# Kernel optimization log

Hardware: AMD Instinct MI355X
Metric: run time of the kernel (lower is better)

Reference implementation:

```python
import jax, jax.numpy as jnp
import numpy as np


def setup_inputs() -> dict:
    key = jax.random.key(0)
    ks = jax.random.split(key, 8)
    B, S, I, H = 64, 256, 1024, 1024
    stdv = 1.0 / np.sqrt(H)
    inputs = jax.random.normal(ks[0], (B, S, I), dtype=jnp.float32)
    h0 = jax.random.normal(ks[1], (1, B, H), dtype=jnp.float32)
    c0 = jax.random.normal(ks[2], (1, B, H), dtype=jnp.float32)
    # concatenated gate params in order (i, f, g, o), uniform(-stdv, stdv) like reset_weigths
    w_i = jax.random.uniform(ks[3], (4 * H, I), minval=-stdv, maxval=stdv, dtype=jnp.float32)
    w_h = jax.random.uniform(ks[4], (4 * H, H), minval=-stdv, maxval=stdv, dtype=jnp.float32)
    b_i = jax.random.uniform(ks[5], (4 * H,), minval=-stdv, maxval=stdv, dtype=jnp.float32)
    b_h = jax.random.uniform(ks[6], (4 * H,), minval=-stdv, maxval=stdv, dtype=jnp.float32)
    return {"inputs": inputs, "h0": h0, "c0": c0, "w_i": w_i, "w_h": w_h, "b_i": b_i, "b_h": b_h}


def _lstm(inputs, h0, c0, w_i, w_h, b_i, b_h):
    H = w_h.shape[1]
    h, c = h0[0], c0[0]  # (B, H)

    def step(carry, x):
        h, c = carry
        # fused gate GEMMs: (B, 4H)
        gates = x @ w_i.T + b_i + h @ w_h.T + b_h
        i, f, g, o = jnp.split(gates, 4, axis=-1)
        i = jax.nn.sigmoid(i)
        f = jax.nn.sigmoid(f)
        g = jnp.tanh(g)
        o = jax.nn.sigmoid(o)
        c_next = f * c + i * g
        h_next = o * jnp.tanh(c_next)
        return (h_next, c_next), h_next

    xs = jnp.transpose(inputs, (1, 0, 2))  # (S, B, I)
    (h, c), hs = jax.lax.scan(step, (h, c), xs)
    hidden_seq = jnp.transpose(hs, (1, 0, 2))  # (B, S, H)
    return hidden_seq, h[None], c[None]


def reference(inputs, h0, c0, w_i, w_h, b_i, b_h):
    return _lstm(inputs, h0, c0, w_i, w_h, b_i, b_h)
```

## Files before the change

kernel.cpp:

```cpp
#include <hip/hip_runtime.h>
#include <hip/hip_bf16.h>
#include <stdint.h>

typedef __bf16 bf16x8 __attribute__((ext_vector_type(8)));
typedef float f32x4 __attribute__((ext_vector_type(4)));
typedef float f32x2 __attribute__((ext_vector_type(2)));
typedef unsigned short u16;
typedef unsigned short u16x4 __attribute__((ext_vector_type(4)));
typedef unsigned long long u64;

#define B_  64
#define S_  256
#define I_  1024
#define H_  1024
#define NG  4096
#define M_  16384

using gvoid_p = const __attribute__((address_space(1))) void*;
using lvoid_p = __attribute__((address_space(3))) void*;

__device__ __forceinline__ void gl_lds16(const void* g, void* l) {
  __builtin_amdgcn_global_load_lds((gvoid_p)g, (lvoid_p)l, 16, 0, 0);
}

__device__ __forceinline__ u16 f2bf(float f) {
  __hip_bfloat16 h = __float2bfloat16(f);
  union { __hip_bfloat16 h; u16 u; } c; c.h = h; return c.u;
}
__device__ __forceinline__ float bf2f(u16 u) {
  union { unsigned u; float f; } c; c.u = ((unsigned)u) << 16; return c.f;
}

__device__ __forceinline__ u64 ld8(const u64* p) {
  return __hip_atomic_load(p, __ATOMIC_RELAXED, __HIP_MEMORY_SCOPE_AGENT);
}

__global__ void cvt_x(const float* __restrict__ x, u16* __restrict__ xb) {
  int bid = blockIdx.x;
  int b = bid & 63, s = bid >> 6;
  int t = threadIdx.x;
  float4 v = ((const float4*)(x + (size_t)b * (S_ * I_) + (size_t)s * I_))[t];
  u16x4 o;
  o[0] = f2bf(v.x); o[1] = f2bf(v.y); o[2] = f2bf(v.z); o[3] = f2bf(v.w);
  ((u16x4*)(xb + (size_t)bid * I_))[t] = o;
}

__global__ void cvt_w(const float* __restrict__ w, u16* __restrict__ wb) {
  size_t i = ((size_t)blockIdx.x * 256 + threadIdx.x) * 4;
  float4 v = *(const float4*)(w + i);
  u16x4 o;
  o[0] = f2bf(v.x); o[1] = f2bf(v.y); o[2] = f2bf(v.z); o[3] = f2bf(v.w);
  *(u16x4*)(wb + i) = o;
}

__global__ void cvt_w_perm(const float* __restrict__ w, u16* __restrict__ wb) {
  const int r = blockIdx.x;
  const int g = r >> 10, c = r & 1023;
  const int rp = c * 4 + g;
  float4 v = ((const float4*)(w + (size_t)r * I_))[threadIdx.x];
  u16x4 o;
  o[0] = f2bf(v.x); o[1] = f2bf(v.y); o[2] = f2bf(v.z); o[3] = f2bf(v.w);
  ((u16x4*)(wb + (size_t)rp * I_))[threadIdx.x] = o;
}

__global__ __launch_bounds__(256) void gemm_bt(const u16* __restrict__ A,
                                               const u16* __restrict__ BT,
                                               u16* __restrict__ C) {
  __shared__ u16 As[128 * 32];
  __shared__ u16 Bs[128 * 32];
  const int tid  = threadIdx.x;
  const int lane = tid & 63;
  const int wv   = tid >> 6;
  const int wm   = wv & 1, wn = wv >> 1;
  const int quad = lane >> 4, l16 = lane & 15;
  const int m0 = blockIdx.y * 128;
  const int n0 = blockIdx.x * 128;

  const int c0i = tid, c1i = tid + 256;
  const int ar0 = c0i >> 2, ak0 = (c0i & 3) * 8;
  const int ar1 = c1i >> 2, ak1 = (c1i & 3) * 8;

  f32x4 acc[4][4] = {};

  for (int kt = 0; kt < 32; ++kt) {
    const int k0 = kt * 32;
    __syncthreads();
    gl_lds16(A + (size_t)(m0 + ar0) * I_ + k0 + ak0, &As[c0i * 8]);
    gl_lds16(A + (size_t)(m0 + ar1) * I_ + k0 + ak1, &As[c1i * 8]);
    gl_lds16(BT + (size_t)(n0 + ar0) * I_ + k0 + ak0, &Bs[c0i * 8]);
    gl_lds16(BT + (size_t)(n0 + ar1) * I_ + k0 + ak1, &Bs[c1i * 8]);
    __syncthreads();

    bf16x8 af[4], bfr[4];
#pragma unroll
    for (int mi = 0; mi < 4; ++mi)
      af[mi] = *(const bf16x8*)&As[(wm * 64 + mi * 16 + l16) * 32 + quad * 8];
#pragma unroll
    for (int ni = 0; ni < 4; ++ni)
      bfr[ni] = *(const bf16x8*)&Bs[(wn * 64 + ni * 16 + l16) * 32 + quad * 8];
#pragma unroll
    for (int mi = 0; mi < 4; ++mi)
#pragma unroll
      for (int ni = 0; ni < 4; ++ni)
        acc[mi][ni] = __builtin_amdgcn_mfma_f32_16x16x32_bf16(af[mi], bfr[ni], acc[mi][ni], 0, 0, 0);
  }

#pragma unroll
  for (int mi = 0; mi < 4; ++mi)
#pragma unroll
    for (int ni = 0; ni < 4; ++ni) {
      const int col = n0 + wn * 64 + ni * 16 + l16;
#pragma unroll
      for (int r = 0; r < 4; ++r) {
        const int row = m0 + wm * 64 + mi * 16 + quad * 4 + r;
        C[(size_t)row * NG + col] = f2bf(acc[mi][ni][r]);
      }
    }
}

__global__ __launch_bounds__(256, 1) void lstm_rec(
    const u16* __restrict__ whb,
    const u16* __restrict__ gxp,
    const float* __restrict__ b_i, const float* __restrict__ b_h,
    const float* __restrict__ h0, const float* __restrict__ c0,
    u16* hbuf,
    float* __restrict__ out,
    unsigned* flags) {
  const int tid = threadIdx.x, lane = tid & 63, v = tid >> 6;
  const int quad = lane >> 4, l16 = lane & 15;
  const int blk = blockIdx.x;
  const int q = blk & 3, cg4 = blk >> 2;
  const int colbase = cg4 * 16 + v * 4;
  const int row = q * 16 + l16;
  const int col = colbase + quad;

  __shared__ __align__(16) u16 hs[16 * 1024];

  float cst = c0[(size_t)row * H_ + col];
  float hl  = h0[(size_t)row * H_ + col];

  {
    unsigned hu = (unsigned)f2bf(hl);
    float ha = __shfl_down(hl, 16);
    unsigned p = hu | ((unsigned)f2bf(ha) << 16);
    unsigned p2 = __shfl_down(p, 32);
    if (quad == 0) {
      u64 pp = (u64)p | ((u64)p2 << 32);
      __hip_atomic_store((u64*)(hbuf + (size_t)row * H_ + colbase), pp,
                         __ATOMIC_RELAXED, __HIP_MEMORY_SCOPE_AGENT);
    }
  }
  __syncthreads();
  if (tid == 0)
    __hip_atomic_store(&flags[q * 64 + cg4], 1u,
                       __ATOMIC_RELAXED, __HIP_MEMORY_SCOPE_AGENT);

  f32x4 bias;
#pragma unroll
  for (int r = 0; r < 4; ++r)
    bias[r] = b_i[r * H_ + col] + b_h[r * H_ + col];

  const int wrow = (l16 & 3) * H_ + colbase + (l16 >> 2);
  bf16x8 wf[32];
#pragma unroll
  for (int kt = 0; kt < 32; ++kt) {
    const u64* wp = (const u64*)(whb + (size_t)wrow * H_ + kt * 32 + quad * 8);
    union { u64 u[2]; bf16x8 v; } c;
    c.u[0] = ld8(wp);
    c.u[1] = ld8(wp + 1);
    wf[kt] = c.v;
  }

  const unsigned* fl = flags + q * 64;
  const char* hsb = (const char*)hs;
  const int swz = (l16 & 7) << 4;

#pragma unroll 1
  for (int s = 0; s < S_; ++s) {
    u16x4 gx4 = *(const u16x4*)(gxp + (size_t)(s * 64 + row) * NG + col * 4);

    {
      const unsigned tgt = (unsigned)(s + 1);
      while (1) {
        unsigned f = __hip_atomic_load(fl + lane, __ATOMIC_RELAXED, __HIP_MEMORY_SCOPE_AGENT);
        if (__all((int)(f >= tgt))) break;
        __builtin_amdgcn_s_sleep(1);
      }
    }

    {
      const u64* src = (const u64*)(hbuf + (size_t)(s & 1) * (B_ * H_)
                                         + (size_t)(q * 16 + v * 4) * H_);
      u64 stg[16];
#pragma unroll
      for (int i = 0; i < 4; ++i)
#pragma unroll
        for (int j = 0; j < 4; ++j)
          stg[i * 4 + j] = ld8(src + (size_t)i * 256 + j * 64 + lane);
#pragma unroll
      for (int i = 0; i < 4; ++i) {
        const int r = v * 4 + i;
#pragma unroll
        for (int j = 0; j < 4; ++j) {
          const int c = (j * 64 + lane) * 8;
          *(u64*)((char*)hs + r * 2048 + (c ^ ((r & 7) << 4))) = stg[i * 4 + j];
        }
      }
    }
    __syncthreads();

    f32x4 acc[4] = {};
#pragma unroll
    for (int kt = 0; kt < 32; ++kt) {
      bf16x8 bv = *(const bf16x8*)(hsb + l16 * 2048 + ((kt * 64 + quad * 16) ^ swz));
      acc[kt & 3] = __builtin_amdgcn_mfma_f32_16x16x32_bf16(wf[kt], bv, acc[kt & 3], 0, 0, 0);
    }

    f32x4 g4;
#pragma unroll
    for (int r = 0; r < 4; ++r)
      g4[r] = acc[0][r] + acc[1][r] + acc[2][r] + acc[3][r]
            + bias[r] + bf2f(gx4[r]);

    float iv = 1.f / (1.f + __expf(-g4[0]));
    float fv = 1.f / (1.f + __expf(-g4[1]));
    float gz = fminf(fmaxf(g4[2], -15.f), 15.f);
    float eg = __expf(2.f * gz);
    float gv = (eg - 1.f) / (eg + 1.f);
    float ov = 1.f / (1.f + __expf(-g4[3]));
    float cn = fv * cst + iv * gv;
    cst = cn;
    float cc = fminf(fmaxf(cn, -15.f), 15.f);
    float ec = __expf(2.f * cc);
    hl = ov * ((ec - 1.f) / (ec + 1.f));

    unsigned hu = (unsigned)f2bf(hl);
    float ha = __shfl_down(hl, 16);
    unsigned p = hu | ((unsigned)f2bf(ha) << 16);
    unsigned p2 = __shfl_down(p, 32);
    float o2 = __shfl_down(hl, 32);
    float o3 = __shfl_down(ha, 32);

    if (quad == 0) {
      u64 pp = (u64)p | ((u64)p2 << 32);
      __hip_atomic_store(
          (u64*)(hbuf + (size_t)((s + 1) & 1) * (B_ * H_)
                      + (size_t)row * H_ + colbase),
          pp, __ATOMIC_RELAXED, __HIP_MEMORY_SCOPE_AGENT);
    }
    __syncthreads();
    if (tid == 0)
      __hip_atomic_store(&flags[q * 64 + cg4], (unsigned)(s + 2),
                         __ATOMIC_RELAXED, __HIP_MEMORY_SCOPE_AGENT);
    if (quad == 0) {
      f32x4 ovv = { hl, ha, o2, o3 };
      __builtin_nontemporal_store(ovv,
          (f32x4*)(out + ((size_t)row * S_ + s) * H_ + colbase));
    }
  }

  {
    const size_t base = (size_t)B_ * S_ * H_;
    out[base + (size_t)row * H_ + col] = hl;
    out[base + (size_t)B_ * H_ + (size_t)row * H_ + col] = cst;
  }
}

extern "C" void kernel_launch(void* const* d_in, const int* in_sizes, int n_in,
                              void* d_out, int out_size, void* d_ws, size_t ws_size,
                              hipStream_t stream) {
  const float* x  = (const float*)d_in[0];
  const float* h0 = (const float*)d_in[1];
  const float* c0 = (const float*)d_in[2];
  const float* wi = (const float*)d_in[3];
  const float* wh = (const float*)d_in[4];
  const float* bi = (const float*)d_in[5];
  const float* bh = (const float*)d_in[6];
  float* out = (float*)d_out;

  char* ws = (char*)d_ws;
  u16* xb   = (u16*)(ws);
  u16* wib  = (u16*)(ws + 33554432);
  u16* whb  = (u16*)(ws + 41943040);
  u16* gxp  = (u16*)(ws + 50331648);
  u16* hbuf = (u16*)(ws + 184549376);
  unsigned* flags = (unsigned*)(ws + 184811520);

  cvt_x<<<M_, 256, 0, stream>>>(x, xb);
  cvt_w_perm<<<NG, 256, 0, stream>>>(wi, wib);
  cvt_w<<<4096, 256, 0, stream>>>(wh, whb);
  gemm_bt<<<dim3(NG / 128, M_ / 128), 256, 0, stream>>>(xb, wib, gxp);
  (void)hipMemsetAsync(flags, 0, 1024, stream);

  void* args[] = { &whb, &gxp, &bi, &bh, &h0, &c0, &hbuf, &out, &flags };
  (void)hipLaunchCooperativeKernel((void*)lstm_rec, dim3(256), dim3(256), args, 0, stream);
}
```

Measured before the change: 1.484 ms.

## Replace flag barrier with tagged hidden-state words and double-buffered LDS

Each hidden-state word now carries its step tag in its upper 32 bits, so consumers poll the data directly instead of a separate flag array. This removes the per-step __syncthreads plus flag store and the flag spin on the producer side. The kernel also moves to 128 blocks of 512 threads with double-buffered LDS, so one barrier per step suffices, and the output store is no longer nontemporal. The costs are doubled global traffic for the exchanged state and retry loads while polling. The tag buffer reuses the xb workspace region, which is dead once the GEMM has run.

```diff
diff --git a/kernel.cpp b/kernel.cpp
--- a/kernel.cpp
+++ b/kernel.cpp
@@ -4,9 +4,9 @@
 
 typedef __bf16 bf16x8 __attribute__((ext_vector_type(8)));
 typedef float f32x4 __attribute__((ext_vector_type(4)));
-typedef float f32x2 __attribute__((ext_vector_type(2)));
 typedef unsigned short u16;
 typedef unsigned short u16x4 __attribute__((ext_vector_type(4)));
+typedef unsigned int u32;
 typedef unsigned long long u64;
 
 #define B_  64
@@ -118,23 +118,22 @@
     }
 }
 
-__global__ __launch_bounds__(256, 1) void lstm_rec(
+__global__ __launch_bounds__(512, 2) void lstm_rec(
     const u16* __restrict__ whb,
     const u16* __restrict__ gxp,
     const float* __restrict__ b_i, const float* __restrict__ b_h,
     const float* __restrict__ h0, const float* __restrict__ c0,
-    u16* hbuf,
-    float* __restrict__ out,
-    unsigned* flags) {
+    u64* tb,
+    float* __restrict__ out) {
   const int tid = threadIdx.x, lane = tid & 63, v = tid >> 6;
   const int quad = lane >> 4, l16 = lane & 15;
   const int blk = blockIdx.x;
-  const int q = blk & 3, cg4 = blk >> 2;
-  const int colbase = cg4 * 16 + v * 4;
+  const int q = blk & 3, cg = blk >> 2;
+  const int colbase = cg * 32 + v * 4;
   const int row = q * 16 + l16;
   const int col = colbase + quad;
 
-  __shared__ __align__(16) u16 hs[16 * 1024];
+  __shared__ __align__(16) u16 hs[2 * 16 * 1024];
 
   float cst = c0[(size_t)row * H_ + col];
   float hl  = h0[(size_t)row * H_ + col];
@@ -142,18 +141,14 @@
   {
     unsigned hu = (unsigned)f2bf(hl);
     float ha = __shfl_down(hl, 16);
-    unsigned p = hu | ((unsigned)f2bf(ha) << 16);
-    unsigned p2 = __shfl_down(p, 32);
-    if (quad == 0) {
-      u64 pp = (u64)p | ((u64)p2 << 32);
-      __hip_atomic_store((u64*)(hbuf + (size_t)row * H_ + colbase), pp,
+    unsigned lo = hu | ((unsigned)f2bf(ha) << 16);
+    if ((quad & 1) == 0) {
+      const int unit = cg * 16 + v * 2 + (quad >> 1);
+      __hip_atomic_store(tb + (size_t)row * 512 + unit,
+                         ((u64)1u << 32) | (u64)lo,
                          __ATOMIC_RELAXED, __HIP_MEMORY_SCOPE_AGENT);
     }
   }
-  __syncthreads();
-  if (tid == 0)
-    __hip_atomic_store(&flags[q * 64 + cg4], 1u,
-                       __ATOMIC_RELAXED, __HIP_MEMORY_SCOPE_AGENT);
 
   f32x4 bias;
 #pragma unroll
@@ -171,7 +166,6 @@
     wf[kt] = c.v;
   }
 
-  const unsigned* fl = flags + q * 64;
   const char* hsb = (const char*)hs;
   const int swz = (l16 & 7) << 4;
 
@@ -179,31 +173,37 @@
   for (int s = 0; s < S_; ++s) {
     u16x4 gx4 = *(const u16x4*)(gxp + (size_t)(s * 64 + row) * NG + col * 4);
 
+    const u64* src = tb + (size_t)(s & 1) * (64 * 512)
+                   + (size_t)(q * 16 + v * 2) * 512;
+    u64 stg[2][8];
+#pragma unroll
+    for (int i = 0; i < 2; ++i)
+#pragma unroll
+      for (int j = 0; j < 8; ++j)
+        stg[i][j] = ld8(src + (size_t)i * 512 + j * 64 + lane);
+    const unsigned tag = (unsigned)(s + 1);
+    while (1) {
+      unsigned bad = 0;
+#pragma unroll
+      for (int i = 0; i < 2; ++i)
+#pragma unroll
+        for (int j = 0; j < 8; ++j)
+          if ((unsigned)(stg[i][j] >> 32) != tag) {
+            bad = 1;
+            stg[i][j] = ld8(src + (size_t)i * 512 + j * 64 + lane);
+          }
+      if (!__any((int)bad)) break;
+    }
     {
-      const unsigned tgt = (unsigned)(s + 1);
-      while (1) {
-        unsigned f = __hip_atomic_load(fl + lane, __ATOMIC_RELAXED, __HIP_MEMORY_SCOPE_AGENT);
-        if (__all((int)(f >= tgt))) break;
-        __builtin_amdgcn_s_sleep(1);
-      }
-    }
-
-    {
-      const u64* src = (const u64*)(hbuf + (size_t)(s & 1) * (B_ * H_)
-                                         + (size_t)(q * 16 + v * 4) * H_);
-      u64 stg[16];
-#pragma unroll
-      for (int i = 0; i < 4; ++i)
-#pragma unroll
-        for (int j = 0; j < 4; ++j)
-          stg[i * 4 + j] = ld8(src + (size_t)i * 256 + j * 64 + lane);
-#pragma unroll
-      for (int i = 0; i < 4; ++i) {
-        const int r = v * 4 + i;
-#pragma unroll
-        for (int j = 0; j < 4; ++j) {
-          const int c = (j * 64 + lane) * 8;
-          *(u64*)((char*)hs + r * 2048 + (c ^ ((r & 7) << 4))) = stg[i * 4 + j];
+      char* dst = (char*)hs + (size_t)(s & 1) * 32768;
+#pragma unroll
+      for (int i = 0; i < 2; ++i) {
+        const int r = v * 2 + i;
+#pragma unroll
+        for (int j = 0; j < 8; ++j) {
+          const int u = j * 64 + lane;
+          *(u32*)(dst + (size_t)r * 2048 + ((u * 4) ^ ((r & 7) << 4))) =
+              (unsigned)stg[i][j];
         }
       }
     }
@@ -212,7 +212,8 @@
     f32x4 acc[4] = {};
 #pragma unroll
     for (int kt = 0; kt < 32; ++kt) {
-      bf16x8 bv = *(const bf16x8*)(hsb + l16 * 2048 + ((kt * 64 + quad * 16) ^ swz));
+      bf16x8 bv = *(const bf16x8*)(hsb + (size_t)(s & 1) * 32768
+                                   + l16 * 2048 + ((kt * 64 + quad * 16) ^ swz));
       acc[kt & 3] = __builtin_amdgcn_mfma_f32_16x16x32_bf16(wf[kt], bv, acc[kt & 3], 0, 0, 0);
     }
 
@@ -236,26 +237,19 @@
 
     unsigned hu = (unsigned)f2bf(hl);
     float ha = __shfl_down(hl, 16);
-    unsigned p = hu | ((unsigned)f2bf(ha) << 16);
-    unsigned p2 = __shfl_down(p, 32);
+    unsigned lo = hu | ((unsigned)f2bf(ha) << 16);
     float o2 = __shfl_down(hl, 32);
     float o3 = __shfl_down(ha, 32);
-
-    if (quad == 0) {
-      u64 pp = (u64)p | ((u64)p2 << 32);
-      __hip_atomic_store(
-          (u64*)(hbuf + (size_t)((s + 1) & 1) * (B_ * H_)
-                      + (size_t)row * H_ + colbase),
-          pp, __ATOMIC_RELAXED, __HIP_MEMORY_SCOPE_AGENT);
-    }
-    __syncthreads();
-    if (tid == 0)
-      __hip_atomic_store(&flags[q * 64 + cg4], (unsigned)(s + 2),
+    if ((quad & 1) == 0) {
+      const int unit = cg * 16 + v * 2 + (quad >> 1);
+      __hip_atomic_store(tb + (size_t)(((s + 1) & 1)) * (64 * 512)
+                            + (size_t)row * 512 + unit,
+                         ((u64)(unsigned)(s + 2) << 32) | (u64)lo,
                          __ATOMIC_RELAXED, __HIP_MEMORY_SCOPE_AGENT);
+    }
     if (quad == 0) {
       f32x4 ovv = { hl, ha, o2, o3 };
-      __builtin_nontemporal_store(ovv,
-          (f32x4*)(out + ((size_t)row * S_ + s) * H_ + colbase));
+      *(f32x4*)(out + ((size_t)row * S_ + s) * H_ + colbase) = ovv;
     }
   }
 
@@ -283,15 +277,14 @@
   u16* wib  = (u16*)(ws + 33554432);
   u16* whb  = (u16*)(ws + 41943040);
   u16* gxp  = (u16*)(ws + 50331648);
-  u16* hbuf = (u16*)(ws + 184549376);
-  unsigned* flags = (unsigned*)(ws + 184811520);
+  u64* tb   = (u64*)(ws);
 
   cvt_x<<<M_, 256, 0, stream>>>(x, xb);
   cvt_w_perm<<<NG, 256, 0, stream>>>(wi, wib);
   cvt_w<<<4096, 256, 0, stream>>>(wh, whb);
   gemm_bt<<<dim3(NG / 128, M_ / 128), 256, 0, stream>>>(xb, wib, gxp);
-  (void)hipMemsetAsync(flags, 0, 1024, stream);
-
-  void* args[] = { &whb, &gxp, &bi, &bh, &h0, &c0, &hbuf, &out, &flags };
-  (void)hipLaunchCooperativeKernel((void*)lstm_rec, dim3(256), dim3(256), args, 0, stream);
-}
+  (void)hipMemsetAsync(tb, 0, 2 * 64 * 512 * sizeof(u64), stream);
+
+  void* args[] = { &whb, &gxp, &bi, &bh, &h0, &c0, &tb, &out };
+  (void)hipLaunchCooperativeKernel((void*)lstm_rec, dim3(128), dim3(512), args, 0, stream);
+}
```

New measurement: 2.500 ms. +68.5%, slower.
